# Optimization experiments

Measured on AMD Instinct MI355X. Metric: run time of the kernel, lower is better.

## Reference

```python
import jax, jax.numpy as jnp
import numpy as np

B, C, H, W = 8, 256, 96, 96
SH = SW = 8            # down_scale window
NHEADS = 8
HD = C // NHEADS       # 32
SCALE = HD ** -0.5


def setup_inputs() -> dict:
    key = jax.random.key(0)
    ks = jax.random.split(key, 9)
    s = 0.02
    return {
        "x": jax.random.normal(ks[0], (B, C, H, W), jnp.float32),
        "Wq": jax.random.normal(ks[1], (C, C), jnp.float32) * s,
        "Wkv": jax.random.normal(ks[2], (2 * C, C), jnp.float32) * s,
        "pool_w": jax.random.normal(ks[3], (C, C, SH, SW), jnp.float32) * s,
        "pool_b": jax.random.normal(ks[4], (C,), jnp.float32) * s,
        "rpe_w": jax.random.normal(ks[5], (C, 1, 3, 3), jnp.float32) * s,
        "rpe_b": jax.random.normal(ks[6], (C,), jnp.float32) * s,
        "proj_w": jax.random.normal(ks[7], (C, C), jnp.float32) * s,
        "proj_b": jax.random.normal(ks[8], (C,), jnp.float32) * s,
    }


def reference(x, Wq, Wkv, pool_w, pool_b, rpe_w, rpe_b, proj_w, proj_b):
    b, c, h, w = x.shape
    nHw, nWw = h // SH, w // SW
    L = nHw * nWw            # number of windows per image
    N = b * L                # total windows
    Q = SH * SW              # queries per window

    # partition (torch unfold with kernel=stride=window) -> [N, SH, SW, C]
    xw = x.reshape(b, c, nHw, SH, nWw, SW).transpose(0, 2, 4, 3, 5, 1)
    xw = xw.reshape(N, SH, SW, c)

    # sub-window pooling: full-window conv == weighted sum over window -> [B, L, C]
    pool_x = (jnp.einsum('nijc,ocij->no', xw, pool_w) + pool_b).reshape(b, L, c)

    # Q projection (no bias): [N, Q, nh, hd] -> [N, nh, Q, hd]
    q = (xw.reshape(N, Q, c) @ Wq.T).reshape(N, Q, NHEADS, HD).transpose(0, 2, 1, 3)
    q = q * SCALE

    # KV projection on pooled tokens (no bias): k, v [B, nh, L, hd]
    kv = (pool_x @ Wkv.T).reshape(b, L, 2, NHEADS, HD)
    k = kv[:, :, 0].transpose(0, 2, 1, 3)
    v = kv[:, :, 1].transpose(0, 2, 1, 3)
    # original tiles pool_x cat-style: window n uses KV of batch (n % B).
    # reshape q to groups g of size B: n = g*B + bb  -> [L, B, nh, Q, hd]
    qg = q.reshape(L, b, NHEADS, Q, HD)
    attn = jnp.einsum('gbhqd,bhkd->gbhqk', qg, k)       # [L, B, nh, Q, L]
    attn = jax.nn.softmax(attn, axis=-1)
    out = jnp.einsum('gbhqk,bhkd->gbhqd', attn, v)      # [L, B, nh, Q, hd]

    # faithful raw reshape: [N, nh, Q, hd] -> (N, Q, nh, hd) -> (B, C, H, W)
    out = out.reshape(N, NHEADS, Q, HD).transpose(0, 2, 1, 3).reshape(b, c, h, w)

    # depthwise 3x3 RPE on original x
    rpe = jax.lax.conv_general_dilated(
        x, rpe_w, window_strides=(1, 1), padding='SAME',
        feature_group_count=c,
        dimension_numbers=('NCHW', 'OIHW', 'NCHW')) + rpe_b[None, :, None, None]

    out = out + rpe
    y = out.reshape(b, -1, c) @ proj_w.T + proj_b       # [B, H*W, C]
    return y
```

## Files before the change

kernel.cpp:

```cpp
#include <hip/hip_runtime.h>
#include <math.h>

#define CB 8
#define CC 256
#define CH 96
#define CWD 96
#define CL 144
#define CN 1152
#define CQ 64
#define NHEADS 8
#define HD 32
#define HWSZ (CH*CWD)
#define QSCALE 0.17677669529663687f
#define NSLICE 32

typedef __attribute__((ext_vector_type(4))) float  f32x4;
typedef __attribute__((ext_vector_type(4))) short  s16x4;
typedef __attribute__((ext_vector_type(8))) short  s16x8;
typedef __attribute__((ext_vector_type(8))) __bf16 bf16x8;

static __device__ __forceinline__ short f2b(float f) {
  union { float f; unsigned u; } v; v.f = f;
  unsigned r = (v.u + 0x7fffu + ((v.u >> 16) & 1u)) >> 16;
  return (short)r;
}

static __device__ __forceinline__ bf16x8 pack8(float4 lo, float4 hi) {
  s16x8 p;
  p[0] = f2b(lo.x); p[1] = f2b(lo.y); p[2] = f2b(lo.z); p[3] = f2b(lo.w);
  p[4] = f2b(hi.x); p[5] = f2b(hi.y); p[6] = f2b(hi.z); p[7] = f2b(hi.w);
  return __builtin_bit_cast(bf16x8, p);
}

__global__ __launch_bounds__(256) void k_cvt(const float* __restrict__ s,
                                             short* __restrict__ d, int n8) {
  int i = blockIdx.x * 256 + threadIdx.x;
  if (i >= n8) return;
  const float4* p = (const float4*)s + (size_t)i * 2;
  float4 a = p[0], b = p[1];
  s16x8 o;
  o[0] = f2b(a.x); o[1] = f2b(a.y); o[2] = f2b(a.z); o[3] = f2b(a.w);
  o[4] = f2b(b.x); o[5] = f2b(b.y); o[6] = f2b(b.z); o[7] = f2b(b.w);
  *(s16x8*)(d + (size_t)i * 8) = o;
}

__global__ __launch_bounds__(256) void k_cvtp(const float* __restrict__ pw,
                                              short* __restrict__ pw2) {
  int g = blockIdx.x * 256 + threadIdx.x;
  int kk8 = (g & 3) * 8;
  int o   = (g >> 2) & 255;
  int kc  = (g >> 10) & 15;
  int ks  = g >> 14;
  int kglob = ks * 512 + kc * 32 + kk8;
  const float* src = pw + (size_t)o * 16384 + kglob;
  float4 a = *(const float4*)src, b = *(const float4*)(src + 4);
  s16x8 oo;
  oo[0] = f2b(a.x); oo[1] = f2b(a.y); oo[2] = f2b(a.z); oo[3] = f2b(a.w);
  oo[4] = f2b(b.x); oo[5] = f2b(b.y); oo[6] = f2b(b.z); oo[7] = f2b(b.w);
  *(s16x8*)(pw2 + (size_t)g * 8) = oo;
}

__global__ __launch_bounds__(256) void k_pool(const float* __restrict__ x,
                                              const short* __restrict__ pw2,
                                              float* __restrict__ part) {
  const int t = threadIdx.x, lane = t & 63, w = t >> 6;
  const int col = lane & 15, quad = lane >> 4;
  const int mb = blockIdx.x, nh = blockIdx.y, ks = blockIdx.z;
  const int wdx = mb * 64 + w * 16 + col;
  const int b = wdx / CL, l = wdx - b * CL;
  const int wh = l / 12, ww = l - wh * 12;
  const size_t xbase = (size_t)b * CC * HWSZ + wh * 8 * CWD + ww * 8;

  f32x4 acc[8] = {};

#pragma unroll 4
  for (int kc = 0; kc < 16; ++kc) {
    const int c = ks * 8 + (kc >> 1);
    const int i = (kc & 1) * 4 + quad;
    const float* ap = x + xbase + (size_t)c * HWSZ + i * CWD;
    bf16x8 af = pack8(*(const float4*)ap, *(const float4*)(ap + 4));
    const short* bk = pw2 + ((size_t)(ks * 16 + kc) * 256 + nh * 128) * 32;
#pragma unroll
    for (int ot = 0; ot < 8; ++ot) {
      s16x8 rb = *(const s16x8*)(bk + (ot * 16 + col) * 32 + quad * 8);
      acc[ot] = __builtin_amdgcn_mfma_f32_16x16x32_bf16(
          af, __builtin_bit_cast(bf16x8, rb), acc[ot], 0, 0, 0);
    }
  }

  float* pp = part + ((size_t)ks * CN + mb * 64 + w * 16) * CC + nh * 128;
#pragma unroll
  for (int ot = 0; ot < 8; ++ot)
#pragma unroll
    for (int r = 0; r < 4; ++r)
      pp[(quad * 4 + r) * CC + ot * 16 + col] = acc[ot][r];
}

__global__ __launch_bounds__(256) void k_poolred(const float* __restrict__ part,
                                                 const float* __restrict__ pbv,
                                                 float* __restrict__ pxr) {
  int base = (blockIdx.x * 256 + threadIdx.x) * 4;
  int m = base & 255;
  float4 s = *(const float4*)&pbv[m];
#pragma unroll
  for (int ss = 0; ss < NSLICE; ++ss) {
    float4 p = *(const float4*)&part[(size_t)ss * (CN * CC) + base];
    s.x += p.x; s.y += p.y; s.z += p.z; s.w += p.w;
  }
  *(float4*)&pxr[base] = s;
}

__global__ __launch_bounds__(256) void k_kv(const float* __restrict__ pxr,
                                            const float* __restrict__ wkv,
                                            float* __restrict__ kbuf,
                                            float* __restrict__ vbuf) {
  const int t = threadIdx.x, tx = t & 15, ty = t >> 4;
  const int row0 = blockIdx.x * 64;
  const int col0 = blockIdx.y * 64;
  __shared__ float As[16][68];
  __shared__ float Bs[16][68];
  float acc[4][4] = {};
  const int ml = t & 15, rB = t >> 4;

  for (int mc = 0; mc < 16; ++mc) {
#pragma unroll
    for (int u = 0; u < 4; ++u) {
      int r = rB + 16 * u;
      As[ml][r] = pxr[(row0 + r) * CC + mc * 16 + ml];
      Bs[ml][r] = wkv[(col0 + r) * CC + mc * 16 + ml];
    }
    __syncthreads();
#pragma unroll
    for (int kk = 0; kk < 16; ++kk) {
      float4 a4 = *(const float4*)&As[kk][ty * 4];
      float4 b4 = *(const float4*)&Bs[kk][tx * 4];
      float av[4] = {a4.x, a4.y, a4.z, a4.w};
      float bv[4] = {b4.x, b4.y, b4.z, b4.w};
#pragma unroll
      for (int ri = 0; ri < 4; ++ri)
#pragma unroll
        for (int cj = 0; cj < 4; ++cj) acc[ri][cj] += av[ri] * bv[cj];
    }
    __syncthreads();
  }

#pragma unroll
  for (int ri = 0; ri < 4; ++ri) {
    int row = row0 + ty * 4 + ri;
    int b = row / CL, l = row - b * CL;
    int j = col0 + tx * 4;
    int d = j & 31, h = (j >> 5) & 7, tkv = j >> 8;
    float* dst = (tkv ? vbuf : kbuf) + ((size_t)(b * NHEADS + h) * CL + l) * HD + d;
    *(float4*)dst = make_float4(acc[ri][0], acc[ri][1], acc[ri][2], acc[ri][3]);
  }
}

__global__ __launch_bounds__(256) void k_q(const float* __restrict__ x,
                                           const short* __restrict__ wqb,
                                           float* __restrict__ qout) {
  const int t = threadIdx.x, lane = t & 63, w = t >> 6;
  const int col = lane & 15, quad = lane >> 4;
  const int n = blockIdx.x;
  const int b = n / CL, l = n - b * CL;
  const int wh = l / 12, ww = l - wh * 12;
  const size_t xwin = (size_t)b * CC * HWSZ + wh * 8 * CWD + ww * 8;

  __shared__ short xq[64][264];
  {
    const int ci = t & 31, ii = t >> 5;
#pragma unroll
    for (int u = 0; u < 8; ++u) {
      const float* ap = x + xwin + (size_t)(ci + 32 * u) * HWSZ + ii * CWD;
      float4 lo = *(const float4*)ap, hi = *(const float4*)(ap + 4);
      float vals[8] = {lo.x, lo.y, lo.z, lo.w, hi.x, hi.y, hi.z, hi.w};
#pragma unroll
      for (int j = 0; j < 8; ++j) xq[ii * 8 + j][ci + 32 * u] = f2b(vals[j]);
    }
  }
  __syncthreads();

  f32x4 acc[4][4] = {};
  for (int kc = 0; kc < 8; ++kc) {
    bf16x8 af[4];
#pragma unroll
    for (int cht = 0; cht < 4; ++cht) {
      s16x8 r = *(const s16x8*)(wqb + (size_t)(w * 64 + cht * 16 + col) * CC + kc * 32 + quad * 8);
      af[cht] = __builtin_bit_cast(bf16x8, r);
    }
#pragma unroll
    for (int qt = 0; qt < 4; ++qt) {
      s16x8 rb = *(const s16x8*)&xq[qt * 16 + col][kc * 32 + quad * 8];
      bf16x8 bfv = __builtin_bit_cast(bf16x8, rb);
#pragma unroll
      for (int cht = 0; cht < 4; ++cht)
        acc[cht][qt] = __builtin_amdgcn_mfma_f32_16x16x32_bf16(af[cht], bfv, acc[cht][qt], 0, 0, 0);
    }
  }

  float* op = qout + (size_t)n * CQ * CC;
#pragma unroll
  for (int qt = 0; qt < 4; ++qt)
#pragma unroll
    for (int cht = 0; cht < 4; ++cht) {
      f32x4 v = acc[cht][qt];
      *(float4*)&op[(qt * 16 + col) * CC + w * 64 + cht * 16 + quad * 4] =
          make_float4(v[0] * QSCALE, v[1] * QSCALE, v[2] * QSCALE, v[3] * QSCALE);
    }
}

__global__ __launch_bounds__(256) void k_attn(const float* __restrict__ kbuf,
                                              const float* __restrict__ vbuf,
                                              float* __restrict__ S) {
  const int t = threadIdx.x;
  const int wv = t >> 6, lane = t & 63;
  const int col = lane & 15, quad = lane >> 4;
  const int task = blockIdx.x * 4 + wv;
  const int n = task >> 3, h = task & 7;
  const int bb = n & 7;

  const float* kh = kbuf + (size_t)(bb * NHEADS + h) * CL * HD;
  const float* vh = vbuf + (size_t)(bb * NHEADS + h) * CL * HD;
  float* Sn = S + (size_t)n * (CQ * CC) + h * HD;

  bf16x8 ka[9];
#pragma unroll
  for (int lt = 0; lt < 9; ++lt) {
    const float* kr = kh + (lt * 16 + col) * HD + quad * 8;
    ka[lt] = pack8(*(const float4*)kr, *(const float4*)(kr + 4));
  }

  s16x4 vt[2][9];
#pragma unroll
  for (int dt = 0; dt < 2; ++dt)
#pragma unroll
    for (int lc = 0; lc < 9; ++lc) {
      s16x4 p;
#pragma unroll
      for (int j = 0; j < 4; ++j)
        p[j] = f2b(vh[(lc * 16 + quad * 4 + j) * HD + dt * 16 + col]);
      vt[dt][lc] = p;
    }

  const f32x4 zero = {0.f, 0.f, 0.f, 0.f};

#pragma unroll
  for (int qt = 0; qt < 4; ++qt) {
    const float* qr = Sn + (size_t)(qt * 16 + col) * CC + quad * 8;
    bf16x8 qb = pack8(*(const float4*)qr, *(const float4*)(qr + 4));

    f32x4 s[9];
#pragma unroll
    for (int lt = 0; lt < 9; ++lt)
      s[lt] = __builtin_amdgcn_mfma_f32_16x16x32_bf16(ka[lt], qb, zero, 0, 0, 0);

    float mx = s[0][0];
#pragma unroll
    for (int lt = 0; lt < 9; ++lt)
#pragma unroll
      for (int r = 0; r < 4; ++r) mx = fmaxf(mx, s[lt][r]);
    mx = fmaxf(mx, __shfl_xor(mx, 16, 64));
    mx = fmaxf(mx, __shfl_xor(mx, 32, 64));

    float sum = 0.f;
    s16x4 pb[9];
#pragma unroll
    for (int lt = 0; lt < 9; ++lt) {
      s16x4 pp;
#pragma unroll
      for (int r = 0; r < 4; ++r) {
        float e = __expf(s[lt][r] - mx);
        sum += e;
        pp[r] = f2b(e);
      }
      pb[lt] = pp;
    }
    sum += __shfl_xor(sum, 16, 64);
    sum += __shfl_xor(sum, 32, 64);
    const float inv = 1.0f / sum;

    f32x4 o0 = zero, o1 = zero;
#pragma unroll
    for (int lc = 0; lc < 9; ++lc) {
      o0 = __builtin_amdgcn_mfma_f32_16x16x16bf16_1k(vt[0][lc], pb[lc], o0, 0, 0, 0);
      o1 = __builtin_amdgcn_mfma_f32_16x16x16bf16_1k(vt[1][lc], pb[lc], o1, 0, 0, 0);
    }

    float* orow = Sn + (size_t)(qt * 16 + col) * CC;
    *(float4*)&orow[quad * 4] =
        make_float4(o0[0] * inv, o0[1] * inv, o0[2] * inv, o0[3] * inv);
    *(float4*)&orow[16 + quad * 4] =
        make_float4(o1[0] * inv, o1[1] * inv, o1[2] * inv, o1[3] * inv);
  }
}

__global__ __launch_bounds__(256) void k_rpe(const float* __restrict__ x,
                                             const float* __restrict__ rw,
                                             const float* __restrict__ rb,
                                             float* __restrict__ S) {
  const int bc = blockIdx.x;
  const int c = bc & 255;
  const int t = threadIdx.x;
  __shared__ float xs[HWSZ];
  const float* xp = x + (size_t)bc * HWSZ;
  float* sp = S + (size_t)bc * HWSZ;
#pragma unroll
  for (int u = 0; u < 36; ++u) xs[t + 256 * u] = xp[t + 256 * u];
  float w9[9];
#pragma unroll
  for (int k = 0; k < 9; ++k) w9[k] = rw[c * 9 + k];
  const float bias = rb[c];
  __syncthreads();
  for (int u = 0; u < 36; ++u) {
    int idx = t + 256 * u;
    int hh = idx / 96, ww = idx - hh * 96;
    float s = bias;
#pragma unroll
    for (int di = 0; di < 3; ++di) {
      int h2 = hh + di - 1;
#pragma unroll
      for (int dj = 0; dj < 3; ++dj) {
        int w2 = ww + dj - 1;
        if ((unsigned)h2 < 96u && (unsigned)w2 < 96u)
          s += xs[h2 * 96 + w2] * w9[di * 3 + dj];
      }
    }
    sp[idx] += s;
  }
}

__global__ __launch_bounds__(256) void k_proj(const short* __restrict__ pjwb,
                                              const float* __restrict__ pjb,
                                              float* __restrict__ S) {
  const int t = threadIdx.x, lane = t & 63, w = t >> 6;
  const int col = lane & 15, quad = lane >> 4;
  const size_t row0 = (size_t)blockIdx.x * 64;

  __shared__ short Sl[64][264];
  const float* Sp = S + row0 * CC;
#pragma unroll
  for (int u = 0; u < 16; ++u) {
    int idx = u * 1024 + t * 4;
    float4 v = *(const float4*)&Sp[idx];
    s16x4 pv;
    pv[0] = f2b(v.x); pv[1] = f2b(v.y); pv[2] = f2b(v.z); pv[3] = f2b(v.w);
    *(s16x4*)&Sl[idx >> 8][idx & 255] = pv;
  }
  __syncthreads();

  f32x4 acc[4][4] = {};
  for (int kc = 0; kc < 8; ++kc) {
    bf16x8 bfr[4];
#pragma unroll
    for (int ot = 0; ot < 4; ++ot) {
      s16x8 r = *(const s16x8*)(pjwb + (size_t)(w * 64 + ot * 16 + col) * CC + kc * 32 + quad * 8);
      bfr[ot] = __builtin_bit_cast(bf16x8, r);
    }
#pragma unroll
    for (int mt = 0; mt < 4; ++mt) {
      s16x8 ra = *(const s16x8*)&Sl[mt * 16 + col][kc * 32 + quad * 8];
      bf16x8 af = __builtin_bit_cast(bf16x8, ra);
#pragma unroll
      for (int ot = 0; ot < 4; ++ot)
        acc[mt][ot] = __builtin_amdgcn_mfma_f32_16x16x32_bf16(af, bfr[ot], acc[mt][ot], 0, 0, 0);
    }
  }

  float bias[4];
#pragma unroll
  for (int ot = 0; ot < 4; ++ot) bias[ot] = pjb[w * 64 + ot * 16 + col];
  float* Sw = S + row0 * CC;
#pragma unroll
  for (int mt = 0; mt < 4; ++mt)
#pragma unroll
    for (int ot = 0; ot < 4; ++ot)
#pragma unroll
      for (int r = 0; r < 4; ++r)
        Sw[(mt * 16 + quad * 4 + r) * CC + w * 64 + ot * 16 + col] = acc[mt][ot][r] + bias[ot];
}

extern "C" void kernel_launch(void* const* d_in, const int* in_sizes, int n_in,
                              void* d_out, int out_size, void* d_ws, size_t ws_size,
                              hipStream_t stream) {
  const float* x    = (const float*)d_in[0];
  const float* wq   = (const float*)d_in[1];
  const float* wkv  = (const float*)d_in[2];
  const float* pw   = (const float*)d_in[3];
  const float* pbv  = (const float*)d_in[4];
  const float* rw   = (const float*)d_in[5];
  const float* rb   = (const float*)d_in[6];
  const float* pjw  = (const float*)d_in[7];
  const float* pjb  = (const float*)d_in[8];
  float* out = (float*)d_out;
  float* ws  = (float*)d_ws;

  float* pxr  = ws;
  float* kbuf = pxr + CN * CC;
  float* vbuf = kbuf + CB * NHEADS * CL * HD;
  short* pw2  = (short*)(vbuf + CB * NHEADS * CL * HD);
  short* wqb  = pw2 + 4194304;
  short* pjwb = wqb + 65536;

  float* part = out;

  k_cvtp   <<<2048, 256, 0, stream>>>(pw, pw2);
  k_cvt    <<<32,   256, 0, stream>>>(wq,  wqb,  8192);
  k_cvt    <<<32,   256, 0, stream>>>(pjw, pjwb, 8192);

  k_pool   <<<dim3(18, 2, NSLICE), 256, 0, stream>>>(x, pw2, part);
  k_poolred<<<288,            256, 0, stream>>>(part, pbv, pxr);
  k_kv     <<<dim3(18, 8),    256, 0, stream>>>(pxr, wkv, kbuf, vbuf);
  k_q      <<<CN,             256, 0, stream>>>(x, wqb, out);
  k_attn   <<<2304,           256, 0, stream>>>(kbuf, vbuf, out);
  k_rpe    <<<CB * CC,        256, 0, stream>>>(x, rw, rb, out);
  k_proj   <<<1152,           256, 0, stream>>>(pjwb, pjb, out);
}
```

Before: 442.0 us.

## Use packed bf16 conversion, retile pool GEMM, and give attention one block per window

Replaces the hand-written bf16 rounding with HIP's packed float2-to-bf16 intrinsics in every conversion site. The pool GEMM tile is reshaped so each wave covers two 16-row tiles and 64 output channels, with each weight fragment reused across two MFMAs, which cuts redundant loads of the bf16 pool weight. The attention kernel now launches one 512-thread block per window with one wave per head. The intent is fewer ALU instructions for conversion and more data reuse, at the cost of changed occupancy and grid shapes.

```diff
diff --git a/kernel.cpp b/kernel.cpp
--- a/kernel.cpp
+++ b/kernel.cpp
@@ -1,4 +1,5 @@
 #include <hip/hip_runtime.h>
+#include <hip/hip_bf16.h>
 #include <math.h>
 
 #define CB 8
@@ -20,16 +21,24 @@
 typedef __attribute__((ext_vector_type(8))) __bf16 bf16x8;
 
 static __device__ __forceinline__ short f2b(float f) {
-  union { float f; unsigned u; } v; v.f = f;
-  unsigned r = (v.u + 0x7fffu + ((v.u >> 16) & 1u)) >> 16;
-  return (short)r;
+  __hip_bfloat16 h = __float2bfloat16(f);
+  return __builtin_bit_cast(short, h);
 }
 
 static __device__ __forceinline__ bf16x8 pack8(float4 lo, float4 hi) {
-  s16x8 p;
-  p[0] = f2b(lo.x); p[1] = f2b(lo.y); p[2] = f2b(lo.z); p[3] = f2b(lo.w);
-  p[4] = f2b(hi.x); p[5] = f2b(hi.y); p[6] = f2b(hi.z); p[7] = f2b(hi.w);
-  return __builtin_bit_cast(bf16x8, p);
+  union { __hip_bfloat162 h2[4]; s16x8 v; } u;
+  u.h2[0] = __float22bfloat162_rn(make_float2(lo.x, lo.y));
+  u.h2[1] = __float22bfloat162_rn(make_float2(lo.z, lo.w));
+  u.h2[2] = __float22bfloat162_rn(make_float2(hi.x, hi.y));
+  u.h2[3] = __float22bfloat162_rn(make_float2(hi.z, hi.w));
+  return __builtin_bit_cast(bf16x8, u.v);
+}
+
+static __device__ __forceinline__ s16x4 pack4(float4 v) {
+  union { __hip_bfloat162 h2[2]; s16x4 v; } u;
+  u.h2[0] = __float22bfloat162_rn(make_float2(v.x, v.y));
+  u.h2[1] = __float22bfloat162_rn(make_float2(v.z, v.w));
+  return u.v;
 }
 
 __global__ __launch_bounds__(256) void k_cvt(const float* __restrict__ s,
@@ -37,11 +46,7 @@
   int i = blockIdx.x * 256 + threadIdx.x;
   if (i >= n8) return;
   const float4* p = (const float4*)s + (size_t)i * 2;
-  float4 a = p[0], b = p[1];
-  s16x8 o;
-  o[0] = f2b(a.x); o[1] = f2b(a.y); o[2] = f2b(a.z); o[3] = f2b(a.w);
-  o[4] = f2b(b.x); o[5] = f2b(b.y); o[6] = f2b(b.z); o[7] = f2b(b.w);
-  *(s16x8*)(d + (size_t)i * 8) = o;
+  *(s16x8*)(d + (size_t)i * 8) = __builtin_bit_cast(s16x8, pack8(p[0], p[1]));
 }
 
 __global__ __launch_bounds__(256) void k_cvtp(const float* __restrict__ pw,
@@ -53,11 +58,8 @@
   int ks  = g >> 14;
   int kglob = ks * 512 + kc * 32 + kk8;
   const float* src = pw + (size_t)o * 16384 + kglob;
-  float4 a = *(const float4*)src, b = *(const float4*)(src + 4);
-  s16x8 oo;
-  oo[0] = f2b(a.x); oo[1] = f2b(a.y); oo[2] = f2b(a.z); oo[3] = f2b(a.w);
-  oo[4] = f2b(b.x); oo[5] = f2b(b.y); oo[6] = f2b(b.z); oo[7] = f2b(b.w);
-  *(s16x8*)(pw2 + (size_t)g * 8) = oo;
+  *(s16x8*)(pw2 + (size_t)g * 8) =
+      __builtin_bit_cast(s16x8, pack8(*(const float4*)src, *(const float4*)(src + 4)));
 }
 
 __global__ __launch_bounds__(256) void k_pool(const float* __restrict__ x,
@@ -65,35 +67,48 @@
                                               float* __restrict__ part) {
   const int t = threadIdx.x, lane = t & 63, w = t >> 6;
   const int col = lane & 15, quad = lane >> 4;
-  const int mb = blockIdx.x, nh = blockIdx.y, ks = blockIdx.z;
-  const int wdx = mb * 64 + w * 16 + col;
-  const int b = wdx / CL, l = wdx - b * CL;
-  const int wh = l / 12, ww = l - wh * 12;
-  const size_t xbase = (size_t)b * CC * HWSZ + wh * 8 * CWD + ww * 8;
-
-  f32x4 acc[8] = {};
+  const int mb = blockIdx.x, ks = blockIdx.y;
+
+  size_t xbase[2];
+#pragma unroll
+  for (int rt = 0; rt < 2; ++rt) {
+    int wdx = mb * 32 + rt * 16 + col;
+    int b = wdx / CL, l = wdx - b * CL;
+    int wh = l / 12, ww = l - wh * 12;
+    xbase[rt] = (size_t)b * CC * HWSZ + wh * 8 * CWD + ww * 8;
+  }
+
+  f32x4 acc[2][4] = {};
 
 #pragma unroll 4
   for (int kc = 0; kc < 16; ++kc) {
     const int c = ks * 8 + (kc >> 1);
     const int i = (kc & 1) * 4 + quad;
-    const float* ap = x + xbase + (size_t)c * HWSZ + i * CWD;
-    bf16x8 af = pack8(*(const float4*)ap, *(const float4*)(ap + 4));
-    const short* bk = pw2 + ((size_t)(ks * 16 + kc) * 256 + nh * 128) * 32;
-#pragma unroll
-    for (int ot = 0; ot < 8; ++ot) {
-      s16x8 rb = *(const s16x8*)(bk + (ot * 16 + col) * 32 + quad * 8);
-      acc[ot] = __builtin_amdgcn_mfma_f32_16x16x32_bf16(
-          af, __builtin_bit_cast(bf16x8, rb), acc[ot], 0, 0, 0);
-    }
-  }
-
-  float* pp = part + ((size_t)ks * CN + mb * 64 + w * 16) * CC + nh * 128;
-#pragma unroll
-  for (int ot = 0; ot < 8; ++ot)
-#pragma unroll
-    for (int r = 0; r < 4; ++r)
-      pp[(quad * 4 + r) * CC + ot * 16 + col] = acc[ot][r];
+    bf16x8 af[2];
+#pragma unroll
+    for (int rt = 0; rt < 2; ++rt) {
+      const float* ap = x + xbase[rt] + (size_t)c * HWSZ + i * CWD;
+      af[rt] = pack8(*(const float4*)ap, *(const float4*)(ap + 4));
+    }
+    const short* bk = pw2 + ((size_t)(ks * 16 + kc) * 256 + w * 64) * 32;
+#pragma unroll
+    for (int ct = 0; ct < 4; ++ct) {
+      s16x8 rb = *(const s16x8*)(bk + (ct * 16 + col) * 32 + quad * 8);
+      bf16x8 bf = __builtin_bit_cast(bf16x8, rb);
+#pragma unroll
+      for (int rt = 0; rt < 2; ++rt)
+        acc[rt][ct] = __builtin_amdgcn_mfma_f32_16x16x32_bf16(af[rt], bf, acc[rt][ct], 0, 0, 0);
+    }
+  }
+
+  float* pp = part + ((size_t)ks * CN + mb * 32) * CC + w * 64;
+#pragma unroll
+  for (int rt = 0; rt < 2; ++rt)
+#pragma unroll
+    for (int ct = 0; ct < 4; ++ct)
+#pragma unroll
+      for (int r = 0; r < 4; ++r)
+        pp[(rt * 16 + quad * 4 + r) * CC + ct * 16 + col] = acc[rt][ct][r];
 }
 
 __global__ __launch_bounds__(256) void k_poolred(const float* __restrict__ part,
@@ -208,14 +223,13 @@
     }
 }
 
-__global__ __launch_bounds__(256) void k_attn(const float* __restrict__ kbuf,
+__global__ __launch_bounds__(512) void k_attn(const float* __restrict__ kbuf,
                                               const float* __restrict__ vbuf,
                                               float* __restrict__ S) {
   const int t = threadIdx.x;
-  const int wv = t >> 6, lane = t & 63;
+  const int h = t >> 6, lane = t & 63;
   const int col = lane & 15, quad = lane >> 4;
-  const int task = blockIdx.x * 4 + wv;
-  const int n = task >> 3, h = task & 7;
+  const int n = blockIdx.x;
   const int bb = n & 7;
 
   const float* kh = kbuf + (size_t)(bb * NHEADS + h) * CL * HD;
@@ -234,11 +248,12 @@
   for (int dt = 0; dt < 2; ++dt)
 #pragma unroll
     for (int lc = 0; lc < 9; ++lc) {
-      s16x4 p;
-#pragma unroll
-      for (int j = 0; j < 4; ++j)
-        p[j] = f2b(vh[(lc * 16 + quad * 4 + j) * HD + dt * 16 + col]);
-      vt[dt][lc] = p;
+      float4 vv;
+      vv.x = vh[(lc * 16 + quad * 4 + 0) * HD + dt * 16 + col];
+      vv.y = vh[(lc * 16 + quad * 4 + 1) * HD + dt * 16 + col];
+      vv.z = vh[(lc * 16 + quad * 4 + 2) * HD + dt * 16 + col];
+      vv.w = vh[(lc * 16 + quad * 4 + 3) * HD + dt * 16 + col];
+      vt[dt][lc] = pack4(vv);
     }
 
   const f32x4 zero = {0.f, 0.f, 0.f, 0.f};
@@ -265,14 +280,11 @@
     s16x4 pb[9];
 #pragma unroll
     for (int lt = 0; lt < 9; ++lt) {
-      s16x4 pp;
-#pragma unroll
-      for (int r = 0; r < 4; ++r) {
-        float e = __expf(s[lt][r] - mx);
-        sum += e;
-        pp[r] = f2b(e);
-      }
-      pb[lt] = pp;
+      float4 ev;
+      ev.x = __expf(s[lt][0] - mx); ev.y = __expf(s[lt][1] - mx);
+      ev.z = __expf(s[lt][2] - mx); ev.w = __expf(s[lt][3] - mx);
+      sum += ev.x + ev.y + ev.z + ev.w;
+      pb[lt] = pack4(ev);
     }
     sum += __shfl_xor(sum, 16, 64);
     sum += __shfl_xor(sum, 32, 64);
@@ -341,9 +353,7 @@
   for (int u = 0; u < 16; ++u) {
     int idx = u * 1024 + t * 4;
     float4 v = *(const float4*)&Sp[idx];
-    s16x4 pv;
-    pv[0] = f2b(v.x); pv[1] = f2b(v.y); pv[2] = f2b(v.z); pv[3] = f2b(v.w);
-    *(s16x4*)&Sl[idx >> 8][idx & 255] = pv;
+    *(s16x4*)&Sl[idx >> 8][idx & 255] = pack4(v);
   }
   __syncthreads();
 
@@ -406,11 +416,11 @@
   k_cvt    <<<32,   256, 0, stream>>>(wq,  wqb,  8192);
   k_cvt    <<<32,   256, 0, stream>>>(pjw, pjwb, 8192);
 
-  k_pool   <<<dim3(18, 2, NSLICE), 256, 0, stream>>>(x, pw2, part);
+  k_pool   <<<dim3(36, NSLICE), 256, 0, stream>>>(x, pw2, part);
   k_poolred<<<288,            256, 0, stream>>>(part, pbv, pxr);
   k_kv     <<<dim3(18, 8),    256, 0, stream>>>(pxr, wkv, kbuf, vbuf);
   k_q      <<<CN,             256, 0, stream>>>(x, wqb, out);
-  k_attn   <<<2304,           256, 0, stream>>>(kbuf, vbuf, out);
+  k_attn   <<<CN,             512, 0, stream>>>(kbuf, vbuf, out);
   k_rpe    <<<CB * CC,        256, 0, stream>>>(x, rw, rb, out);
   k_proj   <<<1152,           256, 0, stream>>>(pjwb, pjb, out);
 }
```

After: 451.8 us. 1.02x slower.
